# Performance work log

Hardware: AMD Instinct MI355X
Metric: run time of the kernel (lower is better)

## Reference

```python
import jax, jax.numpy as jnp
import numpy as np

H = 8      # n_heads
HD = 64    # per-head channels (out_channels in __init__, before *= n_heads)


def setup_inputs() -> dict:
    key = jax.random.key(0)
    ks = jax.random.split(key, 10)
    B, C, N = 4, 256, 2048
    O = H * HD
    s = 1.0 / np.sqrt(C).astype(np.float32)
    return {
        "x": jax.random.normal(ks[0], (B, C, N), dtype=jnp.float32),
        "y": jax.random.normal(ks[1], (B, C, N), dtype=jnp.float32),
        "Wq": jax.random.normal(ks[2], (O, C), dtype=jnp.float32) * s,
        "bq": jnp.zeros((O,), dtype=jnp.float32),
        "Wk": jax.random.normal(ks[3], (O, C), dtype=jnp.float32) * s,
        "bk": jnp.zeros((O,), dtype=jnp.float32),
        "Wv": jax.random.normal(ks[4], (O, C), dtype=jnp.float32) * s,
        "bv": jnp.zeros((O,), dtype=jnp.float32),
        "Wp": jax.random.normal(ks[5], (HD, C), dtype=jnp.float32) * s,  # residual projection, bias=False
        "gamma": jax.random.uniform(ks[6], (H, 1, 1, 1), dtype=jnp.float32) + 0.001,
    }


def _conv1x1(W, b, t):
    # 1x1 Conv1d: (O,C) x (B,C,N) -> (B,O,N)
    out = jnp.einsum('oc,bcn->bon', W, t)
    return out if b is None else out + b[None, :, None]


def _heads(t):
    # (B, H*HD, N) -> (H, B, N, HD); channel split into contiguous per-head chunks
    B, _, N = t.shape
    return t.reshape(B, H, HD, N).transpose(1, 0, 3, 2)


def reference(x, y, Wq, bq, Wk, bk, Wv, bv, Wp, gamma):
    # q/k/v projections via 1x1 convs (kernel_size=1, 'stride_effective' padding => same length)
    q = _heads(_conv1x1(Wq, bq, x))   # (H,B,N,HD)
    k = _heads(_conv1x1(Wk, bk, y))   # (H,B,N,HD)
    v = _heads(_conv1x1(Wv, bv, y))   # (H,B,N,HD)

    # energy = bmm(Q, K^T); softmax over last dim (no mask)
    energy = jnp.einsum('hbnd,hbmd->hbnm', q, k)          # (H,B,N,N)
    attn = jax.nn.softmax(energy, axis=-1)

    # out = bmm(attention.transpose(-2,-1), V)  (note the transpose in the original)
    out = jnp.einsum('hbnm,hbnd->hbmd', attn, v)          # (H,B,N,HD)

    # gamma-weighted residual blend with projected y
    yp = _conv1x1(Wp, None, y).transpose(0, 2, 1)         # (B,N,HD)
    g = gamma.reshape(H, 1, 1, 1)
    out = (g * out + yp[None]) / (1.0 + g)                # (H,B,N,HD)
    return out
```

## Files before the change

kernel.cpp:

```cpp
#include <hip/hip_runtime.h>
#include <math.h>

#define B_DIM 4
#define C_DIM 256
#define N_DIM 2048
#define H_DIM 8
#define HD    64
#define HB    32
#define NTOK  (B_DIM * N_DIM)
#define LOG2E 1.44269504f

typedef __attribute__((ext_vector_type(8))) short bf16x8;
typedef __attribute__((ext_vector_type(4))) float f32x4;

static __device__ __forceinline__ short f2bf(float f) {
    unsigned u = __builtin_bit_cast(unsigned, f);
    u += 0x7fffu + ((u >> 16) & 1u);
    return (short)(u >> 16);
}
static __device__ __forceinline__ float bf2f(short s) {
    unsigned u = ((unsigned)(unsigned short)s) << 16;
    return __builtin_bit_cast(float, u);
}
static __device__ __forceinline__ float fx2(float x) {
#if __has_builtin(__builtin_amdgcn_exp2f)
    return __builtin_amdgcn_exp2f(x);
#else
    return exp2f(x);
#endif
}
static __device__ __forceinline__ unsigned pk_bf16(float a, float b) {
#if __has_builtin(__builtin_amdgcn_cvt_pk_bf16_f32)
    auto v = __builtin_amdgcn_cvt_pk_bf16_f32(a, b);
    return __builtin_bit_cast(unsigned, v);
#else
    unsigned ua = __builtin_bit_cast(unsigned, a);
    unsigned ub = __builtin_bit_cast(unsigned, b);
    return ((ua + 0x8000u) >> 16) | ((ub + 0x8000u) & 0xffff0000u);
#endif
}

#define MFMA16(A, Bv, Cv) __builtin_amdgcn_mfma_f32_16x16x32_bf16(A, Bv, Cv, 0, 0, 0)


__global__ __launch_bounds__(256) void cast_all(
    const float* __restrict__ X, const float* __restrict__ Y,
    const float* __restrict__ Wq, const float* __restrict__ Wk,
    const float* __restrict__ Wv, const float* __restrict__ Wp,
    short* __restrict__ XS, short* __restrict__ YS,
    short* __restrict__ WSx, short* __restrict__ WSy)
{
    const int z = blockIdx.z;
    const int t = threadIdx.x;

    if (z == 8) {
        int base = (blockIdx.y * 32 + blockIdx.x) * 256 + t;
#pragma unroll
        for (int rep = 0; rep < 2; ++rep) {
            int gid = base + rep * 32768;
            if (gid >= 51200) break;
            int lane = gid & 63, chunk = gid >> 6;
            int lo = lane & 15, quad = lane >> 4;
            const float* src; short* dst;
            if (chunk < 256) {
                int ot = chunk >> 3, ks = chunk & 7;
                src = Wq + (size_t)(ot * 16 + lo) * C_DIM + ks * 32 + quad * 8;
                dst = WSx + (size_t)chunk * 512 + lane * 8;
            } else {
                int ch = chunk - 256;
                int ot = ch >> 3, ks = ch & 7;
                int row = ot * 16 + lo;
                const float* basep = (row < 512) ? (Wk + (size_t)row * C_DIM)
                                   : (row < 1024) ? (Wv + (size_t)(row - 512) * C_DIM)
                                                  : (Wp + (size_t)(row - 1024) * C_DIM);
                src = basep + ks * 32 + quad * 8;
                dst = WSy + (size_t)ch * 512 + lane * 8;
            }
            bf16x8 o;
#pragma unroll
            for (int j = 0; j < 8; ++j) o[j] = f2bf(src[j]);
            *(bf16x8*)dst = o;
        }
        return;
    }

    const float* src = (z < 4) ? X : Y;
    short* dst = (z < 4) ? XS : YS;
    const int b = z & 3, c0 = blockIdx.y * 64, n0 = blockIdx.x * 64;
    __shared__ float L[64][65];
    for (int i = t; i < 4096; i += 256) {
        int cc = i >> 6, nn = i & 63;
        L[cc][nn] = src[((size_t)b * C_DIM + c0 + cc) * N_DIM + n0 + nn];
    }
    __syncthreads();
#pragma unroll
    for (int half = 0; half < 2; ++half) {
        int cid = half * 256 + t;
        int lane = cid & 63, fi = cid >> 6;
        int ksl = fi & 1, rtl = fi >> 1;
        int lo = lane & 15, quad = lane >> 4;
        bf16x8 o;
#pragma unroll
        for (int j = 0; j < 8; ++j) o[j] = f2bf(L[ksl * 32 + quad * 8 + j][rtl * 16 + lo]);
        int rt = b * 128 + (n0 >> 4) + rtl;
        int ks = (c0 >> 5) + ksl;
        *(bf16x8*)(dst + ((size_t)(rt * 8 + ks) * 64 + lane) * 8) = o;
    }
}

__global__ __launch_bounds__(256) void proj_all(
    const short* __restrict__ WSx, const short* __restrict__ WSy,
    const short* __restrict__ XS, const short* __restrict__ YS,
    const float* __restrict__ bq, const float* __restrict__ bk,
    const float* __restrict__ bv,
    short* __restrict__ QS, short* __restrict__ KS,
    short* __restrict__ VSu, float* __restrict__ Yo)
{
    const int oy = blockIdx.y;
    const bool isq = oy < 8;
    const short* WS = isq ? WSx : WSy;
    const short* Xs = isq ? XS : YS;
    const int oyl = isq ? oy : oy - 8;
    const int o0 = oyl * 64;
    const int tok0 = blockIdx.x * 128;
    const int t = threadIdx.x, wave = t >> 6, lane = t & 63;
    const int lo = lane & 15, quad = lane >> 4;

    __shared__ __align__(16) char smem[34816];

    const int ot = oyl * 4 + wave;
    const int rt0 = tok0 >> 4;
    const f32x4 czero = {0.f, 0.f, 0.f, 0.f};

    f32x4 acc[8];
#pragma unroll
    for (int i = 0; i < 8; ++i) acc[i] = czero;

#pragma unroll 2
    for (int ks = 0; ks < 8; ++ks) {
        bf16x8 a = *(const bf16x8*)(WS + ((size_t)(ot * 8 + ks) * 64 + lane) * 8);
#pragma unroll
        for (int nt = 0; nt < 8; ++nt) {
            bf16x8 bx = *(const bf16x8*)(Xs + ((size_t)((rt0 + nt) * 8 + ks) * 64 + lane) * 8);
            acc[nt] = MFMA16(a, bx, acc[nt]);
        }
    }

    const int b = tok0 >> 11;
    const int n0b = tok0 & (N_DIM - 1);

    if (oy < 16) {
        short* T = (short*)smem;
        const float* bias = isq ? bq : bk;
        const float scale = isq ? LOG2E : 1.f;
        float bvr[4];
#pragma unroll
        for (int r = 0; r < 4; ++r) bvr[r] = bias[o0 + wave * 16 + quad * 4 + r];
#pragma unroll
        for (int nt = 0; nt < 8; ++nt) {
            short4 pk;
            pk.x = f2bf((acc[nt][0] + bvr[0]) * scale);
            pk.y = f2bf((acc[nt][1] + bvr[1]) * scale);
            pk.z = f2bf((acc[nt][2] + bvr[2]) * scale);
            pk.w = f2bf((acc[nt][3] + bvr[3]) * scale);
            *(short4*)(T + (nt * 16 + lo) * 72 + wave * 16 + quad * 4) = pk;
        }
        __syncthreads();
        const int h = oyl;
        const int hb = h * 4 + b;
        short* dst = isq ? QS : KS;
#pragma unroll
        for (int s = 0; s < 4; ++s) {
            int cid = s * 256 + t;
            int ln = cid & 63, fi = cid >> 6;
            int ksd = fi & 1, rtl = fi >> 1;
            bf16x8 v = *(const bf16x8*)(T + (rtl * 16 + (ln & 15)) * 72 + ksd * 32 + (ln >> 4) * 8);
            *(bf16x8*)(dst + (((size_t)(hb * 128 + (n0b >> 4) + rtl) * 2 + ksd) * 512 + ln * 8)) = v;
        }
    } else if (oy < 24) {
        short* T2 = (short*)smem;
        float bvr[4];
#pragma unroll
        for (int r = 0; r < 4; ++r) bvr[r] = bv[o0 - 512 + wave * 16 + quad * 4 + r];
#pragma unroll
        for (int nt = 0; nt < 8; ++nt)
#pragma unroll
            for (int r = 0; r < 4; ++r) {
                int ol = wave * 16 + quad * 4 + r;
                T2[ol * 136 + nt * 16 + lo] = f2bf(acc[nt][r] + bvr[r]);
            }
        __syncthreads();
        const int h = oy - 16;
        const int hb = h * 4 + b;
#pragma unroll
        for (int s = 0; s < 4; ++s) {
            int cid = s * 256 + t;
            int ln = cid & 63, fi = cid >> 6;
            int dt = fi & 3, ksd = (fi >> 2) & 1, nbl = fi >> 3;
            int dl = dt * 16 + (ln & 15);
            int tkl = nbl * 64 + ksd * 32 + (ln >> 4) * 8;
            bf16x8 v = *(const bf16x8*)(T2 + dl * 136 + tkl);
            int nbg = (n0b >> 6) + nbl;
            *(bf16x8*)(VSu + ((size_t)(((hb * 32 + nbg) * 2 + ksd) * 4 + dt) * 64 + ln) * 8) = v;
        }
    } else {
        float* T3 = (float*)smem;
#pragma unroll
        for (int nt = 0; nt < 8; ++nt) {
            float4 f;
            f.x = acc[nt][0]; f.y = acc[nt][1]; f.z = acc[nt][2]; f.w = acc[nt][3];
            *(float4*)(T3 + (nt * 16 + lo) * 68 + wave * 16 + quad * 4) = f;
        }
        __syncthreads();
#pragma unroll
        for (int s = 0; s < 8; ++s) {
            int cid = s * 256 + t;
            int row = cid >> 4, c4 = (cid & 15) * 4;
            float4 f = *(const float4*)(T3 + row * 68 + c4);
            *(float4*)(Yo + ((size_t)(tok0 + row)) * 64 + c4) = f;
        }
    }
}

__global__ __launch_bounds__(256, 4) void rowsum_mfma(
    const short* __restrict__ QS, const short* __restrict__ KS,
    float* __restrict__ RSp)
{
    const int id = blockIdx.x;
    const int hb = ((id & 7) << 2) | ((id >> 3) & 3);
    const int z = (id >> 5) & 1;
    const int n0 = (id >> 6) * 128;
    const int t = threadIdx.x, wave = t >> 6, lane = t & 63;
    const int lo = lane & 15, quad = lane >> 4;
    const f32x4 czero = {0.f, 0.f, 0.f, 0.f};

    bf16x8 a0[2], a1[2];
#pragma unroll
    for (int s = 0; s < 2; ++s) {
        int rt = (n0 >> 4) + s * 4 + wave;
        a0[s] = *(const bf16x8*)(QS + ((size_t)(hb * 128 + rt) * 2 + 0) * 512 + lane * 8);
        a1[s] = *(const bf16x8*)(QS + ((size_t)(hb * 128 + rt) * 2 + 1) * 512 + lane * 8);
    }

    float sm[2][4];
#pragma unroll
    for (int s = 0; s < 2; ++s)
#pragma unroll
        for (int r = 0; r < 4; ++r) sm[s][r] = 0.f;

    const short* kp = KS + ((size_t)(hb * 128) * 2) * 512 + lane * 8
                    + (size_t)z * (N_DIM / 2 / 16) * 2 * 512;
    for (int m0 = 0; m0 < N_DIM / 2; m0 += 64) {
#pragma unroll
        for (int mt = 0; mt < 4; ++mt) {
            bf16x8 b0 = *(const bf16x8*)(kp + (mt * 2 + 0) * 512);
            bf16x8 b1 = *(const bf16x8*)(kp + (mt * 2 + 1) * 512);
#pragma unroll
            for (int s = 0; s < 2; ++s) {
                f32x4 c = MFMA16(a0[s], b0, czero);
                c = MFMA16(a1[s], b1, c);
#pragma unroll
                for (int r = 0; r < 4; ++r) sm[s][r] += fx2(c[r]);
            }
        }
        kp += 8 * 512;
    }

#pragma unroll
    for (int sft = 1; sft < 16; sft <<= 1)
#pragma unroll
        for (int s = 0; s < 2; ++s)
#pragma unroll
            for (int r = 0; r < 4; ++r) sm[s][r] += __shfl_xor(sm[s][r], sft);

    if (lo == 0) {
#pragma unroll
        for (int s = 0; s < 2; ++s) {
            int row = n0 + s * 64 + wave * 16 + quad * 4;
#pragma unroll
            for (int r = 0; r < 4; ++r)
                RSp[((size_t)z * HB + hb) * N_DIM + row + r] = sm[s][r];
        }
    }
}

__global__ __launch_bounds__(256) void v_scale(
    const short* __restrict__ VSu, const float* __restrict__ RSp,
    short* __restrict__ VS)
{
    int t = blockIdx.x * 256 + threadIdx.x;
    int lane = t & 63, fidx = t >> 6;
    int ks = (fidx >> 2) & 1, nb = (fidx >> 3) & 31, hb = fidx >> 8;
    int n = nb * 64 + ks * 32 + (lane >> 4) * 8;
    bf16x8 v = *(const bf16x8*)(VSu + (size_t)t * 8);
    const float* r0 = RSp + (size_t)hb * N_DIM + n;
    const float* r1 = r0 + (size_t)HB * N_DIM;
    bf16x8 o;
#pragma unroll
    for (int j = 0; j < 8; ++j) o[j] = f2bf(bf2f(v[j]) / (r0[j] + r1[j]));
    *(bf16x8*)(VS + (size_t)t * 8) = o;
}

__global__ __launch_bounds__(256, 4) void attnout_mfma(
    const short* __restrict__ QS, const short* __restrict__ KS,
    const short* __restrict__ VS,
    short* __restrict__ PA0, short* __restrict__ PA1)
{
    const int id = blockIdx.x;
    const int hb = ((id & 7) << 2) | ((id >> 3) & 3);
    const int z = (id >> 5) & 1;
    const int m0 = (id >> 6) * 128;

    __shared__ __align__(16) char smem[17408];
    short* Pl = (short*)smem;

    const int t = threadIdx.x, wave = t >> 6, lane = t & 63;
    const int lo = lane & 15, quad = lane >> 4;
    const f32x4 czero = {0.f, 0.f, 0.f, 0.f};

    bf16x8 bk0[2], bk1[2];
#pragma unroll
    for (int s = 0; s < 2; ++s) {
        int rt = (m0 >> 4) + s * 4 + wave;
        bk0[s] = *(const bf16x8*)(KS + ((size_t)(hb * 128 + rt) * 2 + 0) * 512 + lane * 8);
        bk1[s] = *(const bf16x8*)(KS + ((size_t)(hb * 128 + rt) * 2 + 1) * 512 + lane * 8);
    }

    f32x4 oacc[2][4];
#pragma unroll
    for (int s = 0; s < 2; ++s)
#pragma unroll
        for (int dt = 0; dt < 4; ++dt) oacc[s][dt] = czero;

    const short* qp = QS + ((size_t)(hb * 128) * 2) * 512 + lane * 8
                    + (size_t)z * (N_DIM / 2 / 16) * 2 * 512;
    const short* vp = VS + ((size_t)(hb * 32) * 8) * 512 + lane * 8
                    + (size_t)z * (N_DIM / 2 / 64) * 8 * 512;
    short* prowA = Pl + (wave * 16 + lo) * 64;
    short* prowB = prowA + 64 * 64;
    const int lh = lo & 7;
    const int NIT = N_DIM / 2 / 64;

    f32x4 c[4][2];

    {
#pragma unroll
        for (int nt = 0; nt < 4; ++nt) {
            bf16x8 a0 = *(const bf16x8*)(qp + (nt * 2 + 0) * 512);
            bf16x8 a1 = *(const bf16x8*)(qp + (nt * 2 + 1) * 512);
#pragma unroll
            for (int s = 0; s < 2; ++s) {
                c[nt][s] = MFMA16(a0, bk0[s], czero);
                c[nt][s] = MFMA16(a1, bk1[s], c[nt][s]);
            }
        }
        qp += 8 * 512;
    }

    for (int i = 0; i < NIT - 1; ++i) {
        bf16x8 a0[4], a1[4];
#pragma unroll
        for (int nt = 0; nt < 4; ++nt) {
            a0[nt] = *(const bf16x8*)(qp + (nt * 2 + 0) * 512);
            a1[nt] = *(const bf16x8*)(qp + (nt * 2 + 1) * 512);
        }
#pragma unroll
        for (int nt = 0; nt < 4; ++nt)
#pragma unroll
            for (int s = 0; s < 2; ++s) {
                uint2 pk;
                pk.x = pk_bf16(fx2(c[nt][s][0]), fx2(c[nt][s][1]));
                pk.y = pk_bf16(fx2(c[nt][s][2]), fx2(c[nt][s][3]));
                int chunk = nt * 2 + (quad >> 1);
                *(uint2*)((s ? prowB : prowA) + (((chunk ^ lh) << 3) | ((quad & 1) << 2))) = pk;
            }
#pragma unroll
        for (int nt = 0; nt < 4; ++nt)
#pragma unroll
            for (int s = 0; s < 2; ++s) {
                c[nt][s] = MFMA16(a0[nt], bk0[s], czero);
                c[nt][s] = MFMA16(a1[nt], bk1[s], c[nt][s]);
            }
#pragma unroll
        for (int ks = 0; ks < 2; ++ks) {
            bf16x8 ap0 = *(const bf16x8*)(prowA + (((ks * 4 + quad) ^ lh) << 3));
            bf16x8 ap1 = *(const bf16x8*)(prowB + (((ks * 4 + quad) ^ lh) << 3));
#pragma unroll
            for (int dt = 0; dt < 4; ++dt) {
                bf16x8 bv = *(const bf16x8*)(vp + (ks * 4 + dt) * 512);
                oacc[0][dt] = MFMA16(ap0, bv, oacc[0][dt]);
                oacc[1][dt] = MFMA16(ap1, bv, oacc[1][dt]);
            }
        }
        qp += 8 * 512;
        vp += 8 * 512;
    }

#pragma unroll
    for (int nt = 0; nt < 4; ++nt)
#pragma unroll
        for (int s = 0; s < 2; ++s) {
            uint2 pk;
            pk.x = pk_bf16(fx2(c[nt][s][0]), fx2(c[nt][s][1]));
            pk.y = pk_bf16(fx2(c[nt][s][2]), fx2(c[nt][s][3]));
            int chunk = nt * 2 + (quad >> 1);
            *(uint2*)((s ? prowB : prowA) + (((chunk ^ lh) << 3) | ((quad & 1) << 2))) = pk;
        }
#pragma unroll
    for (int ks = 0; ks < 2; ++ks) {
        bf16x8 ap0 = *(const bf16x8*)(prowA + (((ks * 4 + quad) ^ lh) << 3));
        bf16x8 ap1 = *(const bf16x8*)(prowB + (((ks * 4 + quad) ^ lh) << 3));
#pragma unroll
        for (int dt = 0; dt < 4; ++dt) {
            bf16x8 bv = *(const bf16x8*)(vp + (ks * 4 + dt) * 512);
            oacc[0][dt] = MFMA16(ap0, bv, oacc[0][dt]);
            oacc[1][dt] = MFMA16(ap1, bv, oacc[1][dt]);
        }
    }

    short* PA = z ? PA1 : PA0;
    float* T = (float*)smem;
#pragma unroll
    for (int s = 0; s < 2; ++s) {
        __syncthreads();
#pragma unroll
        for (int dt = 0; dt < 4; ++dt)
#pragma unroll
            for (int r = 0; r < 4; ++r)
                T[(wave * 16 + quad * 4 + r) * 68 + dt * 16 + lo] = oacc[s][dt][r];
        __syncthreads();
#pragma unroll
        for (int it = 0; it < 2; ++it) {
            int idx = it * 256 + t;
            int rowl = idx >> 3, dg = (idx & 7) * 8;
            float4 f0 = *(const float4*)(T + rowl * 68 + dg);
            float4 f1 = *(const float4*)(T + rowl * 68 + dg + 4);
            uint4 o;
            o.x = pk_bf16(f0.x, f0.y);
            o.y = pk_bf16(f0.z, f0.w);
            o.z = pk_bf16(f1.x, f1.y);
            o.w = pk_bf16(f1.z, f1.w);
            int m = m0 + s * 64 + rowl;
            *(uint4*)(PA + ((size_t)(hb * N_DIM + m)) * 64 + dg) = o;
        }
    }
}

__global__ __launch_bounds__(256) void combine_out(
    const short* __restrict__ PA0, const short* __restrict__ PA1,
    const float* __restrict__ YP, const float* __restrict__ gamma,
    float* __restrict__ out)
{
    size_t flat = ((size_t)blockIdx.x * 256 + threadIdx.x) * 8;
    int d  = (int)(flat & 63);
    int n  = (int)((flat >> 6) & (N_DIM - 1));
    int hb = (int)(flat >> 17);
    int h = hb >> 2, b = hb & 3;
    float g = gamma[h];
    float inv = 1.f / (1.f + g);
    float gi = g * inv;
    bf16x8 p0 = *(const bf16x8*)(PA0 + flat);
    bf16x8 p1 = *(const bf16x8*)(PA1 + flat);
    const float* yp = YP + ((size_t)b * N_DIM + n) * HD + d;
    float o[8];
#pragma unroll
    for (int j = 0; j < 8; ++j)
        o[j] = gi * (bf2f(p0[j]) + bf2f(p1[j])) + inv * yp[j];
    float4 o0 = {o[0], o[1], o[2], o[3]};
    float4 o1 = {o[4], o[5], o[6], o[7]};
    *(float4*)(out + flat) = o0;
    *(float4*)(out + flat + 4) = o1;
}

extern "C" void kernel_launch(void* const* d_in, const int* in_sizes, int n_in,
                              void* d_out, int out_size, void* d_ws, size_t ws_size,
                              hipStream_t stream) {
    const float* x     = (const float*)d_in[0];
    const float* y     = (const float*)d_in[1];
    const float* Wq    = (const float*)d_in[2];
    const float* bq    = (const float*)d_in[3];
    const float* Wk    = (const float*)d_in[4];
    const float* bk    = (const float*)d_in[5];
    const float* Wv    = (const float*)d_in[6];
    const float* bv    = (const float*)d_in[7];
    const float* Wp    = (const float*)d_in[8];
    const float* gamma = (const float*)d_in[9];
    float* out = (float*)d_out;

    const size_t XEL  = (size_t)B_DIM * C_DIM * N_DIM;
    const size_t QKV  = (size_t)HB * N_DIM * HD;

    short* XS  = (short*)d_ws;
    short* YS  = XS + XEL;
    short* WSx = YS + XEL;
    short* WSy = WSx + 512 * C_DIM;
    short* QS  = WSy + 1088 * C_DIM;
    short* KS  = QS + QKV;
    short* VSu = KS + QKV;
    short* VS  = VSu + QKV;
    float* YPb = (float*)(VS + QKV);
    float* RSp = YPb + (size_t)B_DIM * N_DIM * HD;
    short* PA0 = XS;
    short* PA1 = VSu;

    dim3 blk(256);
    cast_all<<<dim3(N_DIM / 64, C_DIM / 64, 9), blk, 0, stream>>>(
        x, y, Wq, Wk, Wv, Wp, XS, YS, WSx, WSy);

    proj_all<<<dim3(NTOK / 128, 25), blk, 0, stream>>>(
        WSx, WSy, XS, YS, bq, bk, bv, QS, KS, VSu, YPb);

    rowsum_mfma<<<dim3(1024), blk, 0, stream>>>(QS, KS, RSp);
    v_scale<<<dim3(2048), blk, 0, stream>>>(VSu, RSp, VS);
    attnout_mfma<<<dim3(1024), blk, 0, stream>>>(QS, KS, VS, PA0, PA1);
    combine_out<<<dim3(2048), blk, 0, stream>>>(PA0, PA1, YPb, gamma, out);
}
```

Baseline: 192.1 us.

## Split rowsum four ways and halve attnout tile to double grid parallelism

```diff
diff --git a/kernel.cpp b/kernel.cpp
--- a/kernel.cpp
+++ b/kernel.cpp
@@ -222,14 +222,14 @@
     }
 }
 
-__global__ __launch_bounds__(256, 4) void rowsum_mfma(
+__global__ __launch_bounds__(256, 6) void rowsum_mfma(
     const short* __restrict__ QS, const short* __restrict__ KS,
-    float* __restrict__ RSp)
+    float* __restrict__ RSp, float* __restrict__ RSpW)
 {
     const int id = blockIdx.x;
     const int hb = ((id & 7) << 2) | ((id >> 3) & 3);
-    const int z = (id >> 5) & 1;
-    const int n0 = (id >> 6) * 128;
+    const int zq = (id >> 5) & 3;
+    const int n0 = (id >> 7) * 128;
     const int t = threadIdx.x, wave = t >> 6, lane = t & 63;
     const int lo = lane & 15, quad = lane >> 4;
     const f32x4 czero = {0.f, 0.f, 0.f, 0.f};
@@ -249,8 +249,8 @@
         for (int r = 0; r < 4; ++r) sm[s][r] = 0.f;
 
     const short* kp = KS + ((size_t)(hb * 128) * 2) * 512 + lane * 8
-                    + (size_t)z * (N_DIM / 2 / 16) * 2 * 512;
-    for (int m0 = 0; m0 < N_DIM / 2; m0 += 64) {
+                    + (size_t)zq * (N_DIM / 4 / 16) * 2 * 512;
+    for (int m0 = 0; m0 < N_DIM / 4; m0 += 64) {
 #pragma unroll
         for (int mt = 0; mt < 4; ++mt) {
             bf16x8 b0 = *(const bf16x8*)(kp + (mt * 2 + 0) * 512);
@@ -274,34 +274,39 @@
             for (int r = 0; r < 4; ++r) sm[s][r] += __shfl_xor(sm[s][r], sft);
 
     if (lo == 0) {
+        float* dst = (zq < 2) ? (RSp  + (size_t)zq * HB * N_DIM)
+                              : (RSpW + (size_t)(zq - 2) * HB * N_DIM);
 #pragma unroll
         for (int s = 0; s < 2; ++s) {
             int row = n0 + s * 64 + wave * 16 + quad * 4;
 #pragma unroll
             for (int r = 0; r < 4; ++r)
-                RSp[((size_t)z * HB + hb) * N_DIM + row + r] = sm[s][r];
+                dst[(size_t)hb * N_DIM + row + r] = sm[s][r];
         }
     }
 }
 
 __global__ __launch_bounds__(256) void v_scale(
     const short* __restrict__ VSu, const float* __restrict__ RSp,
-    short* __restrict__ VS)
+    const float* __restrict__ RSpW, short* __restrict__ VS)
 {
     int t = blockIdx.x * 256 + threadIdx.x;
     int lane = t & 63, fidx = t >> 6;
     int ks = (fidx >> 2) & 1, nb = (fidx >> 3) & 31, hb = fidx >> 8;
     int n = nb * 64 + ks * 32 + (lane >> 4) * 8;
     bf16x8 v = *(const bf16x8*)(VSu + (size_t)t * 8);
-    const float* r0 = RSp + (size_t)hb * N_DIM + n;
+    const float* r0 = RSp  + (size_t)hb * N_DIM + n;
     const float* r1 = r0 + (size_t)HB * N_DIM;
+    const float* r2 = RSpW + (size_t)hb * N_DIM + n;
+    const float* r3 = r2 + (size_t)HB * N_DIM;
     bf16x8 o;
 #pragma unroll
-    for (int j = 0; j < 8; ++j) o[j] = f2bf(bf2f(v[j]) / (r0[j] + r1[j]));
+    for (int j = 0; j < 8; ++j)
+        o[j] = f2bf(bf2f(v[j]) / ((r0[j] + r1[j]) + (r2[j] + r3[j])));
     *(bf16x8*)(VS + (size_t)t * 8) = o;
 }
 
-__global__ __launch_bounds__(256, 4) void attnout_mfma(
+__global__ __launch_bounds__(256, 6) void attnout_mfma(
     const short* __restrict__ QS, const short* __restrict__ KS,
     const short* __restrict__ VS,
     short* __restrict__ PA0, short* __restrict__ PA1)
@@ -309,7 +314,7 @@
     const int id = blockIdx.x;
     const int hb = ((id & 7) << 2) | ((id >> 3) & 3);
     const int z = (id >> 5) & 1;
-    const int m0 = (id >> 6) * 128;
+    const int m0 = (id >> 6) * 64;
 
     __shared__ __align__(16) char smem[17408];
     short* Pl = (short*)smem;
@@ -318,41 +323,34 @@
     const int lo = lane & 15, quad = lane >> 4;
     const f32x4 czero = {0.f, 0.f, 0.f, 0.f};
 
-    bf16x8 bk0[2], bk1[2];
-#pragma unroll
-    for (int s = 0; s < 2; ++s) {
-        int rt = (m0 >> 4) + s * 4 + wave;
-        bk0[s] = *(const bf16x8*)(KS + ((size_t)(hb * 128 + rt) * 2 + 0) * 512 + lane * 8);
-        bk1[s] = *(const bf16x8*)(KS + ((size_t)(hb * 128 + rt) * 2 + 1) * 512 + lane * 8);
-    }
-
-    f32x4 oacc[2][4];
-#pragma unroll
-    for (int s = 0; s < 2; ++s)
-#pragma unroll
-        for (int dt = 0; dt < 4; ++dt) oacc[s][dt] = czero;
+    bf16x8 bk0, bk1;
+    {
+        int rt = (m0 >> 4) + wave;
+        bk0 = *(const bf16x8*)(KS + ((size_t)(hb * 128 + rt) * 2 + 0) * 512 + lane * 8);
+        bk1 = *(const bf16x8*)(KS + ((size_t)(hb * 128 + rt) * 2 + 1) * 512 + lane * 8);
+    }
+
+    f32x4 oacc[4];
+#pragma unroll
+    for (int dt = 0; dt < 4; ++dt) oacc[dt] = czero;
 
     const short* qp = QS + ((size_t)(hb * 128) * 2) * 512 + lane * 8
                     + (size_t)z * (N_DIM / 2 / 16) * 2 * 512;
     const short* vp = VS + ((size_t)(hb * 32) * 8) * 512 + lane * 8
                     + (size_t)z * (N_DIM / 2 / 64) * 8 * 512;
     short* prowA = Pl + (wave * 16 + lo) * 64;
-    short* prowB = prowA + 64 * 64;
     const int lh = lo & 7;
     const int NIT = N_DIM / 2 / 64;
 
-    f32x4 c[4][2];
+    f32x4 c[4];
 
     {
 #pragma unroll
         for (int nt = 0; nt < 4; ++nt) {
             bf16x8 a0 = *(const bf16x8*)(qp + (nt * 2 + 0) * 512);
             bf16x8 a1 = *(const bf16x8*)(qp + (nt * 2 + 1) * 512);
-#pragma unroll
-            for (int s = 0; s < 2; ++s) {
-                c[nt][s] = MFMA16(a0, bk0[s], czero);
-                c[nt][s] = MFMA16(a1, bk1[s], c[nt][s]);
-            }
+            c[nt] = MFMA16(a0, bk0, czero);
+            c[nt] = MFMA16(a1, bk1, c[nt]);
         }
         qp += 8 * 512;
     }
@@ -365,31 +363,27 @@
             a1[nt] = *(const bf16x8*)(qp + (nt * 2 + 1) * 512);
         }
 #pragma unroll
-        for (int nt = 0; nt < 4; ++nt)
-#pragma unroll
-            for (int s = 0; s < 2; ++s) {
-                uint2 pk;
-                pk.x = pk_bf16(fx2(c[nt][s][0]), fx2(c[nt][s][1]));
-                pk.y = pk_bf16(fx2(c[nt][s][2]), fx2(c[nt][s][3]));
-                int chunk = nt * 2 + (quad >> 1);
-                *(uint2*)((s ? prowB : prowA) + (((chunk ^ lh) << 3) | ((quad & 1) << 2))) = pk;
-            }
-#pragma unroll
-        for (int nt = 0; nt < 4; ++nt)
-#pragma unroll
-            for (int s = 0; s < 2; ++s) {
-                c[nt][s] = MFMA16(a0[nt], bk0[s], czero);
-                c[nt][s] = MFMA16(a1[nt], bk1[s], c[nt][s]);
-            }
+        for (int nt = 0; nt < 4; ++nt) {
+            uint2 pk;
+            pk.x = pk_bf16(fx2(c[nt][0]), fx2(c[nt][1]));
+            pk.y = pk_bf16(fx2(c[nt][2]), fx2(c[nt][3]));
+            int chunk = nt * 2 + (quad >> 1);
+            *(uint2*)(prowA + (((chunk ^ lh) << 3) | ((quad & 1) << 2))) = pk;
+        }
+        __builtin_amdgcn_s_setprio(1);
+#pragma unroll
+        for (int nt = 0; nt < 4; ++nt) {
+            c[nt] = MFMA16(a0[nt], bk0, czero);
+            c[nt] = MFMA16(a1[nt], bk1, c[nt]);
+        }
+        __builtin_amdgcn_s_setprio(0);
 #pragma unroll
         for (int ks = 0; ks < 2; ++ks) {
             bf16x8 ap0 = *(const bf16x8*)(prowA + (((ks * 4 + quad) ^ lh) << 3));
-            bf16x8 ap1 = *(const bf16x8*)(prowB + (((ks * 4 + quad) ^ lh) << 3));
 #pragma unroll
             for (int dt = 0; dt < 4; ++dt) {
                 bf16x8 bv = *(const bf16x8*)(vp + (ks * 4 + dt) * 512);
-                oacc[0][dt] = MFMA16(ap0, bv, oacc[0][dt]);
-                oacc[1][dt] = MFMA16(ap1, bv, oacc[1][dt]);
+                oacc[dt] = MFMA16(ap0, bv, oacc[dt]);
             }
         }
         qp += 8 * 512;
@@ -397,52 +391,45 @@
     }
 
 #pragma unroll
-    for (int nt = 0; nt < 4; ++nt)
-#pragma unroll
-        for (int s = 0; s < 2; ++s) {
-            uint2 pk;
-            pk.x = pk_bf16(fx2(c[nt][s][0]), fx2(c[nt][s][1]));
-            pk.y = pk_bf16(fx2(c[nt][s][2]), fx2(c[nt][s][3]));
-            int chunk = nt * 2 + (quad >> 1);
-            *(uint2*)((s ? prowB : prowA) + (((chunk ^ lh) << 3) | ((quad & 1) << 2))) = pk;
-        }
+    for (int nt = 0; nt < 4; ++nt) {
+        uint2 pk;
+        pk.x = pk_bf16(fx2(c[nt][0]), fx2(c[nt][1]));
+        pk.y = pk_bf16(fx2(c[nt][2]), fx2(c[nt][3]));
+        int chunk = nt * 2 + (quad >> 1);
+        *(uint2*)(prowA + (((chunk ^ lh) << 3) | ((quad & 1) << 2))) = pk;
+    }
 #pragma unroll
     for (int ks = 0; ks < 2; ++ks) {
         bf16x8 ap0 = *(const bf16x8*)(prowA + (((ks * 4 + quad) ^ lh) << 3));
-        bf16x8 ap1 = *(const bf16x8*)(prowB + (((ks * 4 + quad) ^ lh) << 3));
 #pragma unroll
         for (int dt = 0; dt < 4; ++dt) {
             bf16x8 bv = *(const bf16x8*)(vp + (ks * 4 + dt) * 512);
-            oacc[0][dt] = MFMA16(ap0, bv, oacc[0][dt]);
-            oacc[1][dt] = MFMA16(ap1, bv, oacc[1][dt]);
+            oacc[dt] = MFMA16(ap0, bv, oacc[dt]);
         }
     }
 
     short* PA = z ? PA1 : PA0;
     float* T = (float*)smem;
-#pragma unroll
-    for (int s = 0; s < 2; ++s) {
-        __syncthreads();
-#pragma unroll
-        for (int dt = 0; dt < 4; ++dt)
-#pragma unroll
-            for (int r = 0; r < 4; ++r)
-                T[(wave * 16 + quad * 4 + r) * 68 + dt * 16 + lo] = oacc[s][dt][r];
-        __syncthreads();
-#pragma unroll
-        for (int it = 0; it < 2; ++it) {
-            int idx = it * 256 + t;
-            int rowl = idx >> 3, dg = (idx & 7) * 8;
-            float4 f0 = *(const float4*)(T + rowl * 68 + dg);
-            float4 f1 = *(const float4*)(T + rowl * 68 + dg + 4);
-            uint4 o;
-            o.x = pk_bf16(f0.x, f0.y);
-            o.y = pk_bf16(f0.z, f0.w);
-            o.z = pk_bf16(f1.x, f1.y);
-            o.w = pk_bf16(f1.z, f1.w);
-            int m = m0 + s * 64 + rowl;
-            *(uint4*)(PA + ((size_t)(hb * N_DIM + m)) * 64 + dg) = o;
-        }
+    __syncthreads();
+#pragma unroll
+    for (int dt = 0; dt < 4; ++dt)
+#pragma unroll
+        for (int r = 0; r < 4; ++r)
+            T[(wave * 16 + quad * 4 + r) * 68 + dt * 16 + lo] = oacc[dt][r];
+    __syncthreads();
+#pragma unroll
+    for (int it = 0; it < 2; ++it) {
+        int idx = it * 256 + t;
+        int rowl = idx >> 3, dg = (idx & 7) * 8;
+        float4 f0 = *(const float4*)(T + rowl * 68 + dg);
+        float4 f1 = *(const float4*)(T + rowl * 68 + dg + 4);
+        uint4 o;
+        o.x = pk_bf16(f0.x, f0.y);
+        o.y = pk_bf16(f0.z, f0.w);
+        o.z = pk_bf16(f1.x, f1.y);
+        o.w = pk_bf16(f1.z, f1.w);
+        int m = m0 + rowl;
+        *(uint4*)(PA + ((size_t)(hb * N_DIM + m)) * 64 + dg) = o;
     }
 }
 
@@ -502,6 +489,7 @@
     float* RSp = YPb + (size_t)B_DIM * N_DIM * HD;
     short* PA0 = XS;
     short* PA1 = VSu;
+    float* RSpW = (float*)WSx;
 
     dim3 blk(256);
     cast_all<<<dim3(N_DIM / 64, C_DIM / 64, 9), blk, 0, stream>>>(
@@ -510,8 +498,8 @@
     proj_all<<<dim3(NTOK / 128, 25), blk, 0, stream>>>(
         WSx, WSy, XS, YS, bq, bk, bv, QS, KS, VSu, YPb);
 
-    rowsum_mfma<<<dim3(1024), blk, 0, stream>>>(QS, KS, RSp);
-    v_scale<<<dim3(2048), blk, 0, stream>>>(VSu, RSp, VS);
-    attnout_mfma<<<dim3(1024), blk, 0, stream>>>(QS, KS, VS, PA0, PA1);
+    rowsum_mfma<<<dim3(2048), blk, 0, stream>>>(QS, KS, RSp, RSpW);
+    v_scale<<<dim3(2048), blk, 0, stream>>>(VSu, RSp, RSpW, VS);
+    attnout_mfma<<<dim3(2048), blk, 0, stream>>>(QS, KS, VS, PA0, PA1);
     combine_out<<<dim3(2048), blk, 0, stream>>>(PA0, PA1, YPb, gamma, out);
 }
```

New measurement: 283.2 us. 1.47x slower.

## Enlarge attention and rowsum tiles to 256 rows, split rowsum over four key quarters

Applied to the files above, without the earlier changes.

```diff
diff --git a/kernel.cpp b/kernel.cpp
--- a/kernel.cpp
+++ b/kernel.cpp
@@ -224,39 +224,39 @@
 
 __global__ __launch_bounds__(256, 4) void rowsum_mfma(
     const short* __restrict__ QS, const short* __restrict__ KS,
-    float* __restrict__ RSp)
+    float* __restrict__ RSp, float* __restrict__ RSpW)
 {
     const int id = blockIdx.x;
     const int hb = ((id & 7) << 2) | ((id >> 3) & 3);
-    const int z = (id >> 5) & 1;
-    const int n0 = (id >> 6) * 128;
+    const int zq = (id >> 5) & 3;
+    const int n0 = (id >> 7) * 256;
     const int t = threadIdx.x, wave = t >> 6, lane = t & 63;
     const int lo = lane & 15, quad = lane >> 4;
     const f32x4 czero = {0.f, 0.f, 0.f, 0.f};
 
-    bf16x8 a0[2], a1[2];
-#pragma unroll
-    for (int s = 0; s < 2; ++s) {
+    bf16x8 a0[4], a1[4];
+#pragma unroll
+    for (int s = 0; s < 4; ++s) {
         int rt = (n0 >> 4) + s * 4 + wave;
         a0[s] = *(const bf16x8*)(QS + ((size_t)(hb * 128 + rt) * 2 + 0) * 512 + lane * 8);
         a1[s] = *(const bf16x8*)(QS + ((size_t)(hb * 128 + rt) * 2 + 1) * 512 + lane * 8);
     }
 
-    float sm[2][4];
-#pragma unroll
-    for (int s = 0; s < 2; ++s)
+    float sm[4][4];
+#pragma unroll
+    for (int s = 0; s < 4; ++s)
 #pragma unroll
         for (int r = 0; r < 4; ++r) sm[s][r] = 0.f;
 
     const short* kp = KS + ((size_t)(hb * 128) * 2) * 512 + lane * 8
-                    + (size_t)z * (N_DIM / 2 / 16) * 2 * 512;
-    for (int m0 = 0; m0 < N_DIM / 2; m0 += 64) {
+                    + (size_t)zq * (N_DIM / 4 / 16) * 2 * 512;
+    for (int m0 = 0; m0 < N_DIM / 4; m0 += 64) {
 #pragma unroll
         for (int mt = 0; mt < 4; ++mt) {
             bf16x8 b0 = *(const bf16x8*)(kp + (mt * 2 + 0) * 512);
             bf16x8 b1 = *(const bf16x8*)(kp + (mt * 2 + 1) * 512);
 #pragma unroll
-            for (int s = 0; s < 2; ++s) {
+            for (int s = 0; s < 4; ++s) {
                 f32x4 c = MFMA16(a0[s], b0, czero);
                 c = MFMA16(a1[s], b1, c);
 #pragma unroll
@@ -269,39 +269,44 @@
 #pragma unroll
     for (int sft = 1; sft < 16; sft <<= 1)
 #pragma unroll
-        for (int s = 0; s < 2; ++s)
+        for (int s = 0; s < 4; ++s)
 #pragma unroll
             for (int r = 0; r < 4; ++r) sm[s][r] += __shfl_xor(sm[s][r], sft);
 
     if (lo == 0) {
-#pragma unroll
-        for (int s = 0; s < 2; ++s) {
+        float* dst = (zq < 2) ? (RSp  + (size_t)zq * HB * N_DIM)
+                              : (RSpW + (size_t)(zq - 2) * HB * N_DIM);
+#pragma unroll
+        for (int s = 0; s < 4; ++s) {
             int row = n0 + s * 64 + wave * 16 + quad * 4;
 #pragma unroll
             for (int r = 0; r < 4; ++r)
-                RSp[((size_t)z * HB + hb) * N_DIM + row + r] = sm[s][r];
+                dst[(size_t)hb * N_DIM + row + r] = sm[s][r];
         }
     }
 }
 
 __global__ __launch_bounds__(256) void v_scale(
     const short* __restrict__ VSu, const float* __restrict__ RSp,
-    short* __restrict__ VS)
+    const float* __restrict__ RSpW, short* __restrict__ VS)
 {
     int t = blockIdx.x * 256 + threadIdx.x;
     int lane = t & 63, fidx = t >> 6;
     int ks = (fidx >> 2) & 1, nb = (fidx >> 3) & 31, hb = fidx >> 8;
     int n = nb * 64 + ks * 32 + (lane >> 4) * 8;
     bf16x8 v = *(const bf16x8*)(VSu + (size_t)t * 8);
-    const float* r0 = RSp + (size_t)hb * N_DIM + n;
+    const float* r0 = RSp  + (size_t)hb * N_DIM + n;
     const float* r1 = r0 + (size_t)HB * N_DIM;
+    const float* r2 = RSpW + (size_t)hb * N_DIM + n;
+    const float* r3 = r2 + (size_t)HB * N_DIM;
     bf16x8 o;
 #pragma unroll
-    for (int j = 0; j < 8; ++j) o[j] = f2bf(bf2f(v[j]) / (r0[j] + r1[j]));
+    for (int j = 0; j < 8; ++j)
+        o[j] = f2bf(bf2f(v[j]) / ((r0[j] + r1[j]) + (r2[j] + r3[j])));
     *(bf16x8*)(VS + (size_t)t * 8) = o;
 }
 
-__global__ __launch_bounds__(256, 4) void attnout_mfma(
+__global__ __launch_bounds__(256, 2) void attnout_mfma(
     const short* __restrict__ QS, const short* __restrict__ KS,
     const short* __restrict__ VS,
     short* __restrict__ PA0, short* __restrict__ PA1)
@@ -309,26 +314,26 @@
     const int id = blockIdx.x;
     const int hb = ((id & 7) << 2) | ((id >> 3) & 3);
     const int z = (id >> 5) & 1;
-    const int m0 = (id >> 6) * 128;
-
-    __shared__ __align__(16) char smem[17408];
+    const int m0 = (id >> 6) * 256;
+
+    __shared__ __align__(16) char smem[32768];
     short* Pl = (short*)smem;
 
     const int t = threadIdx.x, wave = t >> 6, lane = t & 63;
     const int lo = lane & 15, quad = lane >> 4;
     const f32x4 czero = {0.f, 0.f, 0.f, 0.f};
 
-    bf16x8 bk0[2], bk1[2];
-#pragma unroll
-    for (int s = 0; s < 2; ++s) {
+    bf16x8 bk0[4], bk1[4];
+#pragma unroll
+    for (int s = 0; s < 4; ++s) {
         int rt = (m0 >> 4) + s * 4 + wave;
         bk0[s] = *(const bf16x8*)(KS + ((size_t)(hb * 128 + rt) * 2 + 0) * 512 + lane * 8);
         bk1[s] = *(const bf16x8*)(KS + ((size_t)(hb * 128 + rt) * 2 + 1) * 512 + lane * 8);
     }
 
-    f32x4 oacc[2][4];
-#pragma unroll
-    for (int s = 0; s < 2; ++s)
+    f32x4 oacc[4][4];
+#pragma unroll
+    for (int s = 0; s < 4; ++s)
 #pragma unroll
         for (int dt = 0; dt < 4; ++dt) oacc[s][dt] = czero;
 
@@ -336,12 +341,11 @@
                     + (size_t)z * (N_DIM / 2 / 16) * 2 * 512;
     const short* vp = VS + ((size_t)(hb * 32) * 8) * 512 + lane * 8
                     + (size_t)z * (N_DIM / 2 / 64) * 8 * 512;
-    short* prowA = Pl + (wave * 16 + lo) * 64;
-    short* prowB = prowA + 64 * 64;
+    short* prow = Pl + (wave * 16 + lo) * 64;
     const int lh = lo & 7;
     const int NIT = N_DIM / 2 / 64;
 
-    f32x4 c[4][2];
+    f32x4 c[4][4];
 
     {
 #pragma unroll
@@ -349,7 +353,7 @@
             bf16x8 a0 = *(const bf16x8*)(qp + (nt * 2 + 0) * 512);
             bf16x8 a1 = *(const bf16x8*)(qp + (nt * 2 + 1) * 512);
 #pragma unroll
-            for (int s = 0; s < 2; ++s) {
+            for (int s = 0; s < 4; ++s) {
                 c[nt][s] = MFMA16(a0, bk0[s], czero);
                 c[nt][s] = MFMA16(a1, bk1[s], c[nt][s]);
             }
@@ -367,29 +371,34 @@
 #pragma unroll
         for (int nt = 0; nt < 4; ++nt)
 #pragma unroll
-            for (int s = 0; s < 2; ++s) {
+            for (int s = 0; s < 4; ++s) {
                 uint2 pk;
                 pk.x = pk_bf16(fx2(c[nt][s][0]), fx2(c[nt][s][1]));
                 pk.y = pk_bf16(fx2(c[nt][s][2]), fx2(c[nt][s][3]));
                 int chunk = nt * 2 + (quad >> 1);
-                *(uint2*)((s ? prowB : prowA) + (((chunk ^ lh) << 3) | ((quad & 1) << 2))) = pk;
-            }
+                *(uint2*)(prow + s * 4096 + (((chunk ^ lh) << 3) | ((quad & 1) << 2))) = pk;
+            }
+        __builtin_amdgcn_s_setprio(1);
 #pragma unroll
         for (int nt = 0; nt < 4; ++nt)
 #pragma unroll
-            for (int s = 0; s < 2; ++s) {
+            for (int s = 0; s < 4; ++s) {
                 c[nt][s] = MFMA16(a0[nt], bk0[s], czero);
                 c[nt][s] = MFMA16(a1[nt], bk1[s], c[nt][s]);
             }
+        __builtin_amdgcn_s_setprio(0);
 #pragma unroll
         for (int ks = 0; ks < 2; ++ks) {
-            bf16x8 ap0 = *(const bf16x8*)(prowA + (((ks * 4 + quad) ^ lh) << 3));
-            bf16x8 ap1 = *(const bf16x8*)(prowB + (((ks * 4 + quad) ^ lh) << 3));
+            bf16x8 ap[4];
+#pragma unroll
+            for (int s = 0; s < 4; ++s)
+                ap[s] = *(const bf16x8*)(prow + s * 4096 + (((ks * 4 + quad) ^ lh) << 3));
 #pragma unroll
             for (int dt = 0; dt < 4; ++dt) {
                 bf16x8 bv = *(const bf16x8*)(vp + (ks * 4 + dt) * 512);
-                oacc[0][dt] = MFMA16(ap0, bv, oacc[0][dt]);
-                oacc[1][dt] = MFMA16(ap1, bv, oacc[1][dt]);
+#pragma unroll
+                for (int s = 0; s < 4; ++s)
+                    oacc[s][dt] = MFMA16(ap[s], bv, oacc[s][dt]);
             }
         }
         qp += 8 * 512;
@@ -399,29 +408,32 @@
 #pragma unroll
     for (int nt = 0; nt < 4; ++nt)
 #pragma unroll
-        for (int s = 0; s < 2; ++s) {
+        for (int s = 0; s < 4; ++s) {
             uint2 pk;
             pk.x = pk_bf16(fx2(c[nt][s][0]), fx2(c[nt][s][1]));
             pk.y = pk_bf16(fx2(c[nt][s][2]), fx2(c[nt][s][3]));
             int chunk = nt * 2 + (quad >> 1);
-            *(uint2*)((s ? prowB : prowA) + (((chunk ^ lh) << 3) | ((quad & 1) << 2))) = pk;
+            *(uint2*)(prow + s * 4096 + (((chunk ^ lh) << 3) | ((quad & 1) << 2))) = pk;
         }
 #pragma unroll
     for (int ks = 0; ks < 2; ++ks) {
-        bf16x8 ap0 = *(const bf16x8*)(prowA + (((ks * 4 + quad) ^ lh) << 3));
-        bf16x8 ap1 = *(const bf16x8*)(prowB + (((ks * 4 + quad) ^ lh) << 3));
+        bf16x8 ap[4];
+#pragma unroll
+        for (int s = 0; s < 4; ++s)
+            ap[s] = *(const bf16x8*)(prow + s * 4096 + (((ks * 4 + quad) ^ lh) << 3));
 #pragma unroll
         for (int dt = 0; dt < 4; ++dt) {
             bf16x8 bv = *(const bf16x8*)(vp + (ks * 4 + dt) * 512);
-            oacc[0][dt] = MFMA16(ap0, bv, oacc[0][dt]);
-            oacc[1][dt] = MFMA16(ap1, bv, oacc[1][dt]);
+#pragma unroll
+            for (int s = 0; s < 4; ++s)
+                oacc[s][dt] = MFMA16(ap[s], bv, oacc[s][dt]);
         }
     }
 
     short* PA = z ? PA1 : PA0;
     float* T = (float*)smem;
 #pragma unroll
-    for (int s = 0; s < 2; ++s) {
+    for (int s = 0; s < 4; ++s) {
         __syncthreads();
 #pragma unroll
         for (int dt = 0; dt < 4; ++dt)
@@ -502,6 +514,7 @@
     float* RSp = YPb + (size_t)B_DIM * N_DIM * HD;
     short* PA0 = XS;
     short* PA1 = VSu;
+    float* RSpW = (float*)WSx;
 
     dim3 blk(256);
     cast_all<<<dim3(N_DIM / 64, C_DIM / 64, 9), blk, 0, stream>>>(
@@ -510,8 +523,8 @@
     proj_all<<<dim3(NTOK / 128, 25), blk, 0, stream>>>(
         WSx, WSy, XS, YS, bq, bk, bv, QS, KS, VSu, YPb);
 
-    rowsum_mfma<<<dim3(1024), blk, 0, stream>>>(QS, KS, RSp);
-    v_scale<<<dim3(2048), blk, 0, stream>>>(VSu, RSp, VS);
-    attnout_mfma<<<dim3(1024), blk, 0, stream>>>(QS, KS, VS, PA0, PA1);
+    rowsum_mfma<<<dim3(1024), blk, 0, stream>>>(QS, KS, RSp, RSpW);
+    v_scale<<<dim3(2048), blk, 0, stream>>>(VSu, RSp, RSpW, VS);
+    attnout_mfma<<<dim3(512), blk, 0, stream>>>(QS, KS, VS, PA0, PA1);
     combine_out<<<dim3(2048), blk, 0, stream>>>(PA0, PA1, YPb, gamma, out);
 }
```

New measurement: 189.5 us. Within noise of the previous version (-1.4%).
